# Kernel tuning notes

Measured on AMD Instinct MI355X. Metric: run time of the kernel, lower is better.

## Reference

```python
import jax, jax.numpy as jnp
import numpy as np

THRESH = 0.5  # best_threshold from get_best_t('greedy-t', opts)


def setup_inputs() -> dict:
    key = jax.random.key(0)
    B, V, U1 = 4096, 128, 129  # batch, v_size (arriving nodes), u_size + 1 (skip slot at col 0)
    w = jax.random.uniform(key, (B, V, U1), dtype=jnp.float32)
    w = w.at[:, :, 0].set(0.0)  # skip action has zero weight
    return {"weights": w}


def _decode(weights, t):
    # weights: [B, V, U1]; sequential greedy-threshold decoding over the V arriving nodes.
    B, V, U1 = weights.shape

    def step(carry, w_i):
        mask, size = carry            # mask: [B, U1] bool (matched u nodes), size: [B]
        w = jnp.where(mask, 0.0, w_i)  # w[mask] = 0
        w = jnp.where(w < t, 0.0, w)   # threshold: zero weights below t
        fallback = w.sum(axis=1) == 0.0
        w = w.at[:, 0].set(jnp.where(fallback, 1.0, w[:, 0]))  # force skip if nothing passes
        sel = jnp.argmax(w, axis=1)    # [B]
        chosen = jnp.take_along_axis(w_i, sel[:, None], axis=1)[:, 0]  # original edge weight
        onehot = jax.nn.one_hot(sel, U1, dtype=bool).at[:, 0].set(False)  # skip never masked
        return (mask | onehot, size + chosen), sel

    init = (jnp.zeros((B, U1), dtype=bool), jnp.zeros((B,), weights.dtype))
    (mask, size), sels = jax.lax.scan(step, init, jnp.swapaxes(weights, 0, 1))
    # returns (-state.size, sequences) as in the torch module (return_pi=False path)
    return -size, jnp.swapaxes(sels, 0, 1)


def reference(weights):
    return _decode(weights, THRESH)
```

## Files before the change

### kernel.cpp

```cpp
#include <hip/hip_runtime.h>


#define NB 4096
#define NV 128
#define NU1 129
#define WPB 4
#define PD 8

__global__ __launch_bounds__(256)
void greedy_thresh_kernel(const float* __restrict__ w, float* __restrict__ out) {
    const int wave = blockIdx.x * WPB + (threadIdx.x >> 6);
    const int lane = threadIdx.x & 63;

    const float* __restrict__ wb = w + (size_t)wave * (NV * NU1);
    float* __restrict__ out_neg = out;
    float* __restrict__ out_sel = out + NB;

    const int c0 = 1 + lane;
    const int c1 = 65 + lane;
    bool m0 = false, m1 = false;
    float size = 0.0f;
    float s0 = 0.0f, s1 = 0.0f;

    float p0[PD], p1[PD];
    #pragma unroll
    for (int d = 0; d < PD; ++d) {
        p0[d] = wb[d * NU1 + c0];
        p1[d] = wb[d * NU1 + c1];
    }

#define BODY(iexpr, dd, PREFETCH)                                              \
    {                                                                          \
        const int i = (iexpr);                                                 \
        const float v0 = p0[dd], v1 = p1[dd];                                  \
        if (PREFETCH) {                                                        \
            const float* nrow = wb + (size_t)(i + PD) * NU1;                   \
            p0[dd] = nrow[c0];                                                 \
            p1[dd] = nrow[c1];                                                 \
        }                                                                      \
        unsigned k0 = 0u, k1 = 0u;                                             \
        if (!m0 && v0 >= 0.5f)                                                 \
            k0 = ((__float_as_uint(v0) & 0x7FFFFFu) << 8) | (unsigned)(255 - c0); \
        if (!m1 && v1 >= 0.5f)                                                 \
            k1 = ((__float_as_uint(v1) & 0x7FFFFFu) << 8) | (unsigned)(255 - c1); \
        unsigned k = k0 > k1 ? k0 : k1;                                        \
        _Pragma("unroll")                                                      \
        for (int off = 32; off > 0; off >>= 1) {                               \
            unsigned o = __shfl_xor(k, off, 64);                               \
            k = (o > k) ? o : k;                                               \
        }                                                                      \
        int sel = 0;                                                           \
        if (k != 0u) {                                                         \
            sel = 255 - (int)(k & 0xFFu);                                      \
            size += __uint_as_float(0x3F000000u | (k >> 8));                   \
            if (sel == c0) m0 = true;                                          \
            else if (sel == c1) m1 = true;                                     \
        }                                                                      \
        if ((i >> 1) == lane) {                                                \
            if (i & 1) s1 = (float)sel; else s0 = (float)sel;                  \
        }                                                                      \
    }

    for (int ib = 0; ib < NV - PD; ib += PD) {
        #pragma unroll
        for (int d = 0; d < PD; ++d)
            BODY(ib + d, d, true)
    }
    #pragma unroll
    for (int d = 0; d < PD; ++d)
        BODY(NV - PD + d, d, false)

#undef BODY

    float2 sv = make_float2(s0, s1);
    *reinterpret_cast<float2*>(&out_sel[(size_t)wave * NV + 2 * lane]) = sv;
    if (lane == 0) out_neg[wave] = -size;
}

extern "C" void kernel_launch(void* const* d_in, const int* in_sizes, int n_in,
                              void* d_out, int out_size, void* d_ws, size_t ws_size,
                              hipStream_t stream) {
    const float* w = (const float*)d_in[0];
    float* out = (float*)d_out;
    const int blocks = NB / WPB;
    greedy_thresh_kernel<<<blocks, 64 * WPB, 0, stream>>>(w, out);
}
```

Before: 54.67 us.

## Use DPP row_shr/row_bcast max-reduction with readlane and precomputed keys

```diff
diff --git a/kernel.cpp b/kernel.cpp
--- a/kernel.cpp
+++ b/kernel.cpp
@@ -6,6 +6,16 @@
 #define NU1 129
 #define WPB 4
 #define PD 8
+
+__device__ __forceinline__ unsigned mkkey(float v, unsigned inv) {
+    unsigned k = ((__float_as_uint(v) & 0x7FFFFFu) << 8) | inv;
+    return v >= 0.5f ? k : 0u;
+}
+
+#define DPPMAX(x, ctl)                                                         \
+    asm("s_nop 1\n\tv_max_i32_dpp %0, %0, %0 " ctl                             \
+        " row_mask:0xf bank_mask:0xf"                                          \
+        : "+v"(x))
 
 __global__ __launch_bounds__(256)
 void greedy_thresh_kernel(const float* __restrict__ w, float* __restrict__ out) {
@@ -18,7 +28,9 @@
 
     const int c0 = 1 + lane;
     const int c1 = 65 + lane;
-    bool m0 = false, m1 = false;
+    const unsigned inv0 = 255 - c0;
+    const unsigned inv1 = 255 - c1;
+    unsigned keep0 = ~0u, keep1 = ~0u;
     float size = 0.0f;
     float s0 = 0.0f, s1 = 0.0f;
 
@@ -28,47 +40,53 @@
         p0[d] = wb[d * NU1 + c0];
         p1[d] = wb[d * NU1 + c1];
     }
+    unsigned kr0 = mkkey(p0[0], inv0);
+    unsigned kr1 = mkkey(p1[0], inv1);
 
-#define BODY(iexpr, dd, PREFETCH)                                              \
+#define BODY(iexpr, dd, PREF, BLD)                                             \
     {                                                                          \
         const int i = (iexpr);                                                 \
-        const float v0 = p0[dd], v1 = p1[dd];                                  \
-        if (PREFETCH) {                                                        \
+                                                \
+        unsigned ka = kr0 & keep0;                                             \
+        unsigned kb = kr1 & keep1;                                             \
+        int v = (int)(ka > kb ? ka : kb);                                      \
+                                \
+        if (PREF) {                                                            \
             const float* nrow = wb + (size_t)(i + PD) * NU1;                   \
             p0[dd] = nrow[c0];                                                 \
             p1[dd] = nrow[c1];                                                 \
         }                                                                      \
-        unsigned k0 = 0u, k1 = 0u;                                             \
-        if (!m0 && v0 >= 0.5f)                                                 \
-            k0 = ((__float_as_uint(v0) & 0x7FFFFFu) << 8) | (unsigned)(255 - c0); \
-        if (!m1 && v1 >= 0.5f)                                                 \
-            k1 = ((__float_as_uint(v1) & 0x7FFFFFu) << 8) | (unsigned)(255 - c1); \
-        unsigned k = k0 > k1 ? k0 : k1;                                        \
-        _Pragma("unroll")                                                      \
-        for (int off = 32; off > 0; off >>= 1) {                               \
-            unsigned o = __shfl_xor(k, off, 64);                               \
-            k = (o > k) ? o : k;                                               \
+                                    \
+        if (BLD) {                                                             \
+            kr0 = mkkey(p0[(dd + 1) & (PD - 1)], inv0);                        \
+            kr1 = mkkey(p1[(dd + 1) & (PD - 1)], inv1);                        \
         }                                                                      \
-        int sel = 0;                                                           \
-        if (k != 0u) {                                                         \
-            sel = 255 - (int)(k & 0xFFu);                                      \
-            size += __uint_as_float(0x3F000000u | (k >> 8));                   \
-            if (sel == c0) m0 = true;                                          \
-            else if (sel == c1) m1 = true;                                     \
-        }                                                                      \
-        if ((i >> 1) == lane) {                                                \
-            if (i & 1) s1 = (float)sel; else s0 = (float)sel;                  \
-        }                                                                      \
+                          \
+        DPPMAX(v, "row_shr:1");                                                \
+        DPPMAX(v, "row_shr:2");                                                \
+        DPPMAX(v, "row_shr:4");                                                \
+        DPPMAX(v, "row_shr:8");                                                \
+        DPPMAX(v, "row_bcast:15");                                             \
+        DPPMAX(v, "row_bcast:31");                                             \
+        unsigned kk;                                                           \
+        asm("s_nop 1\n\tv_readlane_b32 %0, %1, 63" : "=s"(kk) : "v"(v));       \
+                                                   \
+        const int sel = kk ? (255 - (int)(kk & 0xFFu)) : 0;                    \
+        size += __uint_as_float(kk ? (0x3F000000u | (kk >> 8)) : 0u);          \
+        keep0 = (sel == c0) ? 0u : keep0;                                      \
+        keep1 = (sel == c1) ? 0u : keep1;                                      \
+        const float self = (float)sel;                                         \
+        if ((i >> 1) == lane) { if (i & 1) s1 = self; else s0 = self; }        \
     }
 
     for (int ib = 0; ib < NV - PD; ib += PD) {
         #pragma unroll
         for (int d = 0; d < PD; ++d)
-            BODY(ib + d, d, true)
+            BODY(ib + d, d, true, true)
     }
     #pragma unroll
     for (int d = 0; d < PD; ++d)
-        BODY(NV - PD + d, d, false)
+        BODY(NV - PD + d, d, false, (d < PD - 1))
 
 #undef BODY
 
```

Result: faster. 47.84 us (-12.5%).
